# Kernel optimization log

Hardware: AMD Instinct MI355X
Metric: run time of the kernel (lower is better)

## Reference

```python
import jax, jax.numpy as jnp
import numpy as np

EMBED, HEADS, WIN, UP = 180, 6, 16, 4
HDIM = EMBED // HEADS

def _win_part(x, ws):
    # x: [B, H, W, C] -> [B*(H//ws)*(W//ws), ws, ws, C]
    B, H, W, C = x.shape
    x = x.reshape(B, H // ws, ws, W // ws, ws, C).transpose(0, 1, 3, 2, 4, 5)
    return x.reshape(-1, ws, ws, C)

def _win_rev(w, ws, H, W):
    # inverse of _win_part
    C = w.shape[-1]
    B = w.shape[0] // ((H // ws) * (W // ws))
    x = w.reshape(B, H // ws, W // ws, ws, ws, C).transpose(0, 1, 3, 2, 4, 5)
    return x.reshape(B, H, W, C)

def _ln(x, g, b):
    mu = x.mean(-1, keepdims=True)
    v = ((x - mu) ** 2).mean(-1, keepdims=True)
    return (x - mu) * jax.lax.rsqrt(v + 1e-5) * g + b

def _forward(gumbel_u, x, sel1_w, sel1_b, sel2_w, sel2_b, sel3_w, sel3_b,
             embed_w, embed_b, ln1_g, ln1_b, qkv_w, qkv_b, proj_w, proj_b,
             ln2_g, ln2_b, mlp1_w, mlp1_b, mlp2_w, mlp2_b, up_w, up_b):
    B, C, H, W = x.shape
    ws = H // 4                                     # 64 -> 16 tiles per image
    tiles = _win_part(x.transpose(0, 2, 3, 1), ws)  # [T, ws, ws, C]
    T = tiles.shape[0]
    # --- TileSelection (pooled MLP router) ---
    pooled = tiles.reshape(T, 8, ws // 8, 8, ws // 8, C).mean((2, 4)).reshape(T, 8 * 8 * C)
    f1 = pooled @ sel1_w + sel1_b
    f2 = jax.nn.relu(f1) @ sel2_w + sel2_b
    f3 = jax.nn.relu(f2) @ sel3_w + sel3_b          # [T, 2] routing logits
    # --- hard gumbel-softmax with straight-through estimator (tau=1) ---
    g = -jnp.log(-jnp.log(gumbel_u + 1e-10) + 1e-10)
    y_soft = jax.nn.softmax(f3 + g, axis=-1)
    y_hard = jax.nn.one_hot(jnp.argmax(y_soft, -1), 2, dtype=y_soft.dtype)
    pi = jax.lax.stop_gradient(y_hard - y_soft) + y_soft
    mask = pi[:, 1]                                 # 1 -> transformer expert
    # --- TR expert (SwinIR-style block, dense dispatch over all tiles) ---
    tok = tiles.reshape(T, ws * ws, C) @ embed_w + embed_b   # [T, 4096, 180]
    h = _ln(tok, ln1_g, ln1_b)
    hw = _win_part(h.reshape(T, ws, ws, EMBED), WIN).reshape(-1, WIN * WIN, EMBED)
    Nw, L = hw.shape[0], WIN * WIN
    qkv = (hw @ qkv_w + qkv_b).reshape(Nw, L, 3, HEADS, HDIM)
    q, k, v = qkv[:, :, 0], qkv[:, :, 1], qkv[:, :, 2]
    attn = jax.nn.softmax(jnp.einsum('nlhd,nmhd->nhlm', q, k) / np.sqrt(HDIM).astype(np.float32), axis=-1)
    av = jnp.einsum('nhlm,nmhd->nlhd', attn, v).reshape(Nw, L, EMBED)
    av = av @ proj_w + proj_b
    av = _win_rev(av.reshape(Nw, WIN, WIN, EMBED), WIN, ws, ws).reshape(T, ws * ws, EMBED)
    tok = tok + av
    h2 = _ln(tok, ln2_g, ln2_b)
    tok = tok + jax.nn.gelu(h2 @ mlp1_w + mlp1_b) @ mlp2_w + mlp2_b
    # pixelshuffle x4 upsample: 180 -> 3*4*4
    up = (tok @ up_w + up_b).reshape(T, ws, ws, UP, UP, C)
    up = up.transpose(0, 1, 3, 2, 4, 5).reshape(T, ws * UP, ws * UP, C)
    # --- cheap expert: bicubic x4 ---
    neg = jax.image.resize(tiles, (T, ws * UP, ws * UP, C), method='bicubic')
    # --- combine per-tile and reassemble ---
    m = mask[:, None, None, None]
    sr_tiles = m * up + (1.0 - m) * neg             # [T, 4ws, 4ws, C]
    sr = _win_rev(sr_tiles, H, H * UP, W * UP)      # [B, 4H, 4W, C]
    return sr.transpose(0, 3, 1, 2), f3, f2, f1

def setup_inputs() -> dict:
    key = jax.random.key(0)
    ks = jax.random.split(key, 16)
    B, C, H, W = 1, 3, 256, 256
    T = B * 16
    p = lambda k, s: jax.random.normal(k, s, jnp.float32) * 0.02
    return {
        'x': jax.random.normal(ks[0], (B, C, H, W), jnp.float32),
        'gumbel_u': jax.random.uniform(ks[1], (T, 2), jnp.float32),
        'sel1_w': p(ks[2], (192, 64)), 'sel1_b': jnp.zeros((64,), jnp.float32),
        'sel2_w': p(ks[3], (64, 32)), 'sel2_b': jnp.zeros((32,), jnp.float32),
        'sel3_w': p(ks[4], (32, 2)), 'sel3_b': jnp.zeros((2,), jnp.float32),
        'embed_w': p(ks[5], (3, EMBED)), 'embed_b': jnp.zeros((EMBED,), jnp.float32),
        'ln1_g': jnp.ones((EMBED,), jnp.float32), 'ln1_b': jnp.zeros((EMBED,), jnp.float32),
        'qkv_w': p(ks[6], (EMBED, 3 * EMBED)), 'qkv_b': jnp.zeros((3 * EMBED,), jnp.float32),
        'proj_w': p(ks[7], (EMBED, EMBED)), 'proj_b': jnp.zeros((EMBED,), jnp.float32),
        'ln2_g': jnp.ones((EMBED,), jnp.float32), 'ln2_b': jnp.zeros((EMBED,), jnp.float32),
        'mlp1_w': p(ks[8], (EMBED, 2 * EMBED)), 'mlp1_b': jnp.zeros((2 * EMBED,), jnp.float32),
        'mlp2_w': p(ks[9], (2 * EMBED, EMBED)), 'mlp2_b': jnp.zeros((EMBED,), jnp.float32),
        'up_w': p(ks[10], (EMBED, 3 * UP * UP)), 'up_b': jnp.zeros((3 * UP * UP,), jnp.float32),
    }

def reference(x, gumbel_u, sel1_w, sel1_b, sel2_w, sel2_b, sel3_w, sel3_b,
              embed_w, embed_b, ln1_g, ln1_b, qkv_w, qkv_b, proj_w, proj_b,
              ln2_g, ln2_b, mlp1_w, mlp1_b, mlp2_w, mlp2_b, up_w, up_b):
    return _forward(gumbel_u, x, sel1_w, sel1_b, sel2_w, sel2_b, sel3_w, sel3_b,
                    embed_w, embed_b, ln1_g, ln1_b, qkv_w, qkv_b, proj_w, proj_b,
                    ln2_g, ln2_b, mlp1_w, mlp1_b, mlp2_w, mlp2_b, up_w, up_b)
```

## Files before the change

### kernel.cpp

```cpp
#include <hip/hip_runtime.h>
#include <hip/hip_bf16.h>
#include <cstdint>

typedef __hip_bfloat16 bf16;
typedef __attribute__((ext_vector_type(8))) short short8;
typedef __attribute__((ext_vector_type(4))) short short4v;
typedef __attribute__((ext_vector_type(4))) float f32x4;
typedef __attribute__((ext_vector_type(2))) unsigned int uint2v;

__device__ __forceinline__ float bf2f(bf16 v) { return __bfloat162float(v); }
__device__ __forceinline__ bf16  f2bf(float v) { return __float2bfloat16(v); }
__device__ __forceinline__ float rbf(short s) {
  union { uint32_t u; float f; } c; c.u = ((uint32_t)(uint16_t)s) << 16; return c.f;
}
__device__ __forceinline__ uint32_t pack2(float a, float b) {
  bf16 x = f2bf(a), y = f2bf(b);
  return (uint32_t)(*(uint16_t*)&x) | ((uint32_t)(*(uint16_t*)&y) << 16);
}
__device__ __forceinline__ uint2v pack4(float a, float b, float c, float d) {
  uint2v r; r[0] = pack2(a, b); r[1] = pack2(c, d); return r;
}
__device__ __forceinline__ int swz(int row, int g) { return g ^ (row & 7); }

__device__ __forceinline__ int win_to_token(int m) {
  int n = m >> 8, l = m & 255;
  int t = n >> 4, win = n & 15;
  int wi = win >> 2, wj = win & 3;
  int u = l >> 4, v = l & 15;
  return (t << 12) | ((wi * 16 + u) << 6) | (wj * 16 + v);
}

__global__ __launch_bounds__(256) void k_packsel(
    const float* __restrict__ qkvw, const float* __restrict__ projw,
    const float* __restrict__ mlp1w, const float* __restrict__ mlp2w,
    const float* __restrict__ upw, const float* __restrict__ qkvb,
    bf16* __restrict__ Bt_qkv, bf16* __restrict__ Bt_proj,
    bf16* __restrict__ Bt_mlp1, bf16* __restrict__ Bt_mlp2,
    bf16* __restrict__ Bt_up, float* __restrict__ biasq,
    const float* __restrict__ x, const float* __restrict__ gu,
    const float* __restrict__ s1w, const float* __restrict__ s1b,
    const float* __restrict__ s2w, const float* __restrict__ s2b,
    const float* __restrict__ s3w, const float* __restrict__ s3b,
    float* __restrict__ f1o, float* __restrict__ f2o, float* __restrict__ f3o,
    float* __restrict__ maskp) {
  if (blockIdx.x < 1203) {
    int idx = blockIdx.x * 256 + threadIdx.x;
    const int e0 = 576 * 192, e1 = e0 + 192 * 192, e2 = e1 + 384 * 192,
              e3 = e2 + 192 * 384, e4 = e3 + 64 * 192, e5 = e4 + 576;
    if (idx < e0) {
      int np = idx / 192, k = idx % 192;
      int buf = np / 192, colp = np % 192;
      int hd = colp >> 5, dd = colp & 31;
      float v = 0.f;
      if (dd < 30 && k < 180) v = qkvw[(size_t)k * 540 + buf * 180 + hd * 30 + dd];
      Bt_qkv[idx] = f2bf(v);
    } else if (idx < e1) {
      int off = idx - e0; int n = off / 192, kp = off % 192;
      int hd = kp >> 5, dd = kp & 31;
      float v = (dd < 30 && n < 180) ? projw[(size_t)(hd * 30 + dd) * 180 + n] : 0.f;
      Bt_proj[off] = f2bf(v);
    } else if (idx < e2) {
      int off = idx - e1; int n = off / 192, k = off % 192;
      Bt_mlp1[off] = f2bf((k < 180 && n < 360) ? mlp1w[(size_t)k * 360 + n] : 0.f);
    } else if (idx < e3) {
      int off = idx - e2; int n = off / 384, k = off % 384;
      Bt_mlp2[off] = f2bf((k < 360 && n < 180) ? mlp2w[(size_t)k * 180 + n] : 0.f);
    } else if (idx < e4) {
      int off = idx - e3; int n = off / 192, k = off % 192;
      Bt_up[off] = f2bf((k < 180 && n < 48) ? upw[(size_t)k * 48 + n] : 0.f);
    } else if (idx < e5) {
      int np = idx - e4;
      int buf = np / 192, colp = np % 192;
      int hd = colp >> 5, dd = colp & 31;
      biasq[np] = (dd < 30) ? qkvb[buf * 180 + hd * 30 + dd] : 0.f;
    }
    return;
  }
  int t = blockIdx.x - 1203;
  int tid = threadIdx.x;
  int th = t >> 2, tw = t & 3;
  __shared__ float pooled[192];
  __shared__ float red[256];
  __shared__ float f1s[64], f2s[32], f3s[2];
  if (tid < 192) {
    int ch = tid % 3, j = (tid / 3) & 7, i = tid / 24;
    const float* xp = x + ch * 65536 + (th * 64 + i * 8) * 256 + (tw * 64 + j * 8);
    float s = 0.f;
#pragma unroll
    for (int a = 0; a < 8; ++a)
#pragma unroll
      for (int b = 0; b < 8; ++b) s += xp[a * 256 + b];
    pooled[tid] = s * (1.0f / 64.0f);
  }
  __syncthreads();
  {
    int o = tid & 63, part = tid >> 6;
    float s = 0.f;
    for (int k = part * 48; k < part * 48 + 48; ++k) s = fmaf(pooled[k], s1w[k * 64 + o], s);
    red[tid] = s;
  }
  __syncthreads();
  if (tid < 64) {
    float v = red[tid] + red[tid + 64] + red[tid + 128] + red[tid + 192] + s1b[tid];
    f1o[t * 64 + tid] = v;
    f1s[tid] = fmaxf(v, 0.f);
  }
  __syncthreads();
  {
    int o = tid & 31, part = tid >> 5;
    float s = 0.f;
    for (int k = part * 8; k < part * 8 + 8; ++k) s = fmaf(f1s[k], s2w[k * 32 + o], s);
    red[tid] = s;
  }
  __syncthreads();
  if (tid < 32) {
    float v = s2b[tid];
#pragma unroll
    for (int p = 0; p < 8; ++p) v += red[tid + p * 32];
    f2o[t * 32 + tid] = v;
    f2s[tid] = fmaxf(v, 0.f);
  }
  __syncthreads();
  if (tid < 2) {
    float s = s3b[tid];
    for (int k = 0; k < 32; ++k) s = fmaf(f2s[k], s3w[k * 2 + tid], s);
    f3o[t * 2 + tid] = s;
    f3s[tid] = s;
  }
  __syncthreads();
  if (tid == 0) {
    float g0 = -logf(-logf(gu[t * 2 + 0] + 1e-10f) + 1e-10f);
    float g1 = -logf(-logf(gu[t * 2 + 1] + 1e-10f) + 1e-10f);
    maskp[t] = (f3s[1] + g1 > f3s[0] + g0) ? 1.0f : 0.0f;
  }
}

__global__ __launch_bounds__(256) void k_embed(
    const float* __restrict__ x, const float* __restrict__ ew,
    const float* __restrict__ eb, const float* __restrict__ g1,
    const float* __restrict__ b1, bf16* __restrict__ tok,
    bf16* __restrict__ Aq) {
  int wrow = blockIdx.x * 4 + (threadIdx.x >> 6);
  int lane = threadIdx.x & 63;
  int token = win_to_token(wrow);
  int t = token >> 12, p = token & 4095;
  int r = p >> 6, c = p & 63;
  int gh = (t >> 2) * 64 + r, gw = (t & 3) * 64 + c;
  float x0 = x[gh * 256 + gw];
  float x1 = x[65536 + gh * 256 + gw];
  float x2 = x[131072 + gh * 256 + gw];
  float v[3];
  float s = 0.f, s2 = 0.f;
#pragma unroll
  for (int i = 0; i < 3; ++i) {
    int e = lane + i * 64;
    float vv = 0.f;
    if (e < 180) {
      vv = eb[e];
      vv = fmaf(x0, ew[e], vv);
      vv = fmaf(x1, ew[180 + e], vv);
      vv = fmaf(x2, ew[360 + e], vv);
      tok[(size_t)wrow * 180 + e] = f2bf(vv);
      s += vv; s2 = fmaf(vv, vv, s2);
    }
    v[i] = vv;
  }
#pragma unroll
  for (int off = 32; off; off >>= 1) { s += __shfl_xor(s, off); s2 += __shfl_xor(s2, off); }
  float mu = s * (1.f / 180.f);
  float rs = rsqrtf(s2 * (1.f / 180.f) - mu * mu + 1e-5f);
#pragma unroll
  for (int i = 0; i < 3; ++i) {
    int e = lane + i * 64;
    if (e < 192) {
      float a = (e < 180) ? ((v[i] - mu) * rs * g1[e] + b1[e]) : 0.f;
      Aq[(size_t)wrow * 192 + e] = f2bf(a);
    }
  }
}

__global__ __launch_bounds__(256) void k_qkv2(
    const bf16* __restrict__ A, const bf16* __restrict__ Bt,
    const float* __restrict__ biasq, bf16* __restrict__ Qp,
    bf16* __restrict__ Kp, bf16* __restrict__ Vp) {
  __shared__ bf16 Bs[2][64 * 192];
  const int tid = threadIdx.x;
  const int w = tid >> 6, l = tid & 63;
  const int lr = l & 15, lk = l >> 4;
  const int rbase = blockIdx.x * 128 + w * 32 + lr;

  short8 fa[2][6];
#pragma unroll
  for (int i = 0; i < 2; ++i) {
    const bf16* Ab = A + (size_t)(rbase + i * 16) * 192 + lk * 8;
#pragma unroll
    for (int ks = 0; ks < 6; ++ks) fa[i][ks] = *(const short8*)(Ab + ks * 32);
  }

  {
    const bf16* src = Bt;
#pragma unroll
    for (int it = 0; it < 6; ++it) {
      int c = tid + it * 256;
      int n = c / 24, g = c % 24;
      *(short8*)&Bs[0][n * 192 + swz(n, g) * 8] = *(const short8*)(src + n * 192 + g * 8);
    }
  }

  for (int nt = 0; nt < 9; ++nt) {
    __syncthreads();
    if (nt < 8) {
      const bf16* src = Bt + (size_t)(nt + 1) * 64 * 192;
      bf16* dstb = Bs[(nt + 1) & 1];
#pragma unroll
      for (int it = 0; it < 6; ++it) {
        int c = tid + it * 256;
        int n = c / 24, g = c % 24;
        *(short8*)&dstb[n * 192 + swz(n, g) * 8] = *(const short8*)(src + n * 192 + g * 8);
      }
    }
    const bf16* Bb = Bs[nt & 1];
    f32x4 acc[2][4];
#pragma unroll
    for (int i = 0; i < 2; ++i)
#pragma unroll
      for (int j = 0; j < 4; ++j) acc[i][j] = (f32x4){0.f, 0.f, 0.f, 0.f};
#pragma unroll
    for (int ks = 0; ks < 6; ++ks) {
      short8 fb[4];
#pragma unroll
      for (int j = 0; j < 4; ++j) {
        int rn = j * 16 + lr;
        fb[j] = *(const short8*)&Bb[rn * 192 + swz(rn, ks * 4 + lk) * 8];
      }
#pragma unroll
      for (int i = 0; i < 2; ++i)
#pragma unroll
        for (int j = 0; j < 4; ++j)
          acc[i][j] = __builtin_amdgcn_mfma_f32_16x16x32_bf16(fb[j], fa[i][ks], acc[i][j], 0, 0, 0);
    }
    bf16* dst = (nt < 3) ? Qp : (nt < 6) ? Kp : Vp;
    int c0 = (nt % 3) * 64;
#pragma unroll
    for (int i = 0; i < 2; ++i) {
      int row = rbase + i * 16;
#pragma unroll
      for (int j = 0; j < 4; ++j) {
        int np = nt * 64 + j * 16 + lk * 4;
        f32x4 bv = *(const f32x4*)&biasq[np];
        *(uint2v*)(dst + (size_t)row * 192 + c0 + j * 16 + lk * 4) =
            pack4(acc[i][j][0] + bv[0], acc[i][j][1] + bv[1],
                  acc[i][j][2] + bv[2], acc[i][j][3] + bv[3]);
      }
    }
  }
}

__global__ __launch_bounds__(256) void k_attn2(
    const bf16* __restrict__ Qp, const bf16* __restrict__ Kp,
    const bf16* __restrict__ Vp, bf16* __restrict__ av) {
  const int blk = blockIdx.x;
  const int win = blk / 6, hd = blk % 6;
  const int tid = threadIdx.x;
  const int w = tid >> 6, l = tid & 63;
  const int lr = l & 15, lk = l >> 4;
  const float scale = 0.18257418583505536f;

  __shared__ bf16 Ks[256][40];
  __shared__ bf16 Vs[32][264];
  __shared__ bf16 Ps[4][16][264];

  {
    const bf16* src = Kp + (size_t)(win * 256 + tid) * 192 + hd * 32;
#pragma unroll
    for (int c = 0; c < 4; ++c)
      *(short8*)&Ks[tid][c * 8] = *(const short8*)(src + c * 8);
  }
  {
    const bf16* src = Vp + (size_t)(win * 256 + tid) * 192 + hd * 32;
    short8 vv[4];
#pragma unroll
    for (int c = 0; c < 4; ++c) vv[c] = *(const short8*)(src + c * 8);
#pragma unroll
    for (int c = 0; c < 4; ++c)
#pragma unroll
      for (int e = 0; e < 8; ++e)
        *(short*)&Vs[c * 8 + e][tid] = vv[c][e];
  }
  __syncthreads();

  for (int qt = 0; qt < 4; ++qt) {
    const int qbase = qt * 64 + w * 16;
    short8 fq = *(const short8*)(Qp + (size_t)(win * 256 + qbase + lr) * 192 + hd * 32 + lk * 8);
    f32x4 accS[16];
#pragma unroll
    for (int kt = 0; kt < 16; ++kt) {
      short8 fk = *(const short8*)(&Ks[kt * 16 + lr][lk * 8]);
      accS[kt] = __builtin_amdgcn_mfma_f32_16x16x32_bf16(
          fk, fq, (f32x4){0.f, 0.f, 0.f, 0.f}, 0, 0, 0);
    }
    float mraw = -1e30f;
#pragma unroll
    for (int kt = 0; kt < 16; ++kt)
#pragma unroll
      for (int r = 0; r < 4; ++r) mraw = fmaxf(mraw, accS[kt][r]);
    mraw = fmaxf(mraw, __shfl_xor(mraw, 16));
    mraw = fmaxf(mraw, __shfl_xor(mraw, 32));
    const float mc = mraw * scale;
    float lsum = 0.f;
#pragma unroll
    for (int kt = 0; kt < 16; ++kt) {
      float p0 = __expf(fmaf(accS[kt][0], scale, -mc));
      float p1 = __expf(fmaf(accS[kt][1], scale, -mc));
      float p2 = __expf(fmaf(accS[kt][2], scale, -mc));
      float p3 = __expf(fmaf(accS[kt][3], scale, -mc));
      lsum += (p0 + p1) + (p2 + p3);
      *(uint32_t*)&Ps[w][lr][kt * 16 + lk * 4]     = pack2(p0, p1);
      *(uint32_t*)&Ps[w][lr][kt * 16 + lk * 4 + 2] = pack2(p2, p3);
    }
    lsum += __shfl_xor(lsum, 16);
    lsum += __shfl_xor(lsum, 32);
    __syncthreads();
    f32x4 accO0 = (f32x4){0.f, 0.f, 0.f, 0.f};
    f32x4 accO1 = (f32x4){0.f, 0.f, 0.f, 0.f};
#pragma unroll
    for (int ks = 0; ks < 8; ++ks) {
      short8 fp  = *(const short8*)(&Ps[w][lr][ks * 32 + lk * 8]);
      short8 fv0 = *(const short8*)(&Vs[lr][ks * 32 + lk * 8]);
      short8 fv1 = *(const short8*)(&Vs[16 + lr][ks * 32 + lk * 8]);
      accO0 = __builtin_amdgcn_mfma_f32_16x16x32_bf16(fv0, fp, accO0, 0, 0, 0);
      accO1 = __builtin_amdgcn_mfma_f32_16x16x32_bf16(fv1, fp, accO1, 0, 0, 0);
    }
    float invl = 1.f / lsum;
    bf16* avrow = av + (size_t)(win * 256 + qbase + lr) * 192 + hd * 32;
    *(uint2v*)(avrow + lk * 4) =
        pack4(accO0[0] * invl, accO0[1] * invl, accO0[2] * invl, accO0[3] * invl);
    *(uint2v*)(avrow + 16 + lk * 4) =
        pack4(accO1[0] * invl, accO1[1] * invl, accO1[2] * invl, accO1[3] * invl);
    __syncthreads();
  }
}

__global__ __launch_bounds__(256) void k_post(
    const bf16* __restrict__ av, const bf16* __restrict__ tok,
    const bf16* __restrict__ Btp, const float* __restrict__ pb,
    const float* __restrict__ g2, const float* __restrict__ b2,
    const bf16* __restrict__ Bt1, const float* __restrict__ b1m,
    const bf16* __restrict__ Bt2, const float* __restrict__ b2m,
    const bf16* __restrict__ Btu, const float* __restrict__ bu,
    bf16* __restrict__ up) {
  __shared__ bf16 Bs[2][64 * 192];
  __shared__ bf16 Hm[64 * 192];
  const int tid = threadIdx.x;
  const int w = tid >> 6, l = tid & 63;
  const int lr = l & 15, lk = l >> 4;
  const int row_l = w * 16 + lr;
  const int row_g = blockIdx.x * 64 + row_l;
  const int half = (lk & 1) * 4;

#define STAGE_A(srcp, dstb)                                               \
  {                                                                       \
    const bf16* _s = (srcp);                                              \
    bf16* _d = (dstb);                                                    \
    _Pragma("unroll")                                                     \
    for (int it = 0; it < 6; ++it) {                                      \
      int c = tid + it * 256;                                             \
      int n = c / 24, g = c % 24;                                         \
      *(short8*)&_d[n * 192 + swz(n, g) * 8] =                            \
          *(const short8*)(_s + (size_t)n * 192 + g * 8);                 \
    }                                                                     \
  }
#define STAGE_S(ntv, dstb)                                                \
  {                                                                       \
    bf16* _d = (dstb);                                                    \
    _Pragma("unroll")                                                     \
    for (int it = 0; it < 6; ++it) {                                      \
      int c = tid + it * 256;                                             \
      int n = c / 8, g = c % 8;                                           \
      *(short8*)&_d[n * 64 + swz(n, g) * 8] =                             \
          *(const short8*)(Bt2 + (size_t)n * 384 + (ntv) * 64 + g * 8);   \
    }                                                                     \
  }

  short8 fa[6];
  {
    const bf16* ab = av + (size_t)row_g * 192 + lk * 8;
#pragma unroll
    for (int ks = 0; ks < 6; ++ks) fa[ks] = *(const short8*)(ab + ks * 32);
  }

  f32x4 t2v[3][4];

  STAGE_A(Btp, Bs[0]);

#pragma unroll
  for (int nt = 0; nt < 3; ++nt) {
    __syncthreads();
    if (nt < 2) { STAGE_A(Btp + (size_t)(nt + 1) * 64 * 192, Bs[(nt + 1) & 1]); }
    else        { STAGE_A(Bt1, Bs[1]); }
    const bf16* Bb = Bs[nt & 1];
    f32x4 acc[4];
#pragma unroll
    for (int j = 0; j < 4; ++j) acc[j] = (f32x4){0.f, 0.f, 0.f, 0.f};
#pragma unroll
    for (int ks = 0; ks < 6; ++ks) {
      short8 fb[4];
#pragma unroll
      for (int j = 0; j < 4; ++j) {
        int rn = j * 16 + lr;
        fb[j] = *(const short8*)&Bb[rn * 192 + swz(rn, ks * 4 + lk) * 8];
      }
#pragma unroll
      for (int j = 0; j < 4; ++j)
        acc[j] = __builtin_amdgcn_mfma_f32_16x16x32_bf16(fb[j], fa[ks], acc[j], 0, 0, 0);
    }
#pragma unroll
    for (int j = 0; j < 4; ++j) {
      int n = nt * 64 + j * 16 + lk * 4;
      if (n < 180) {
        f32x4 bv = *(const f32x4*)&pb[n];
        short4v tv = *(const short4v*)(tok + (size_t)row_g * 180 + n);
#pragma unroll
        for (int q = 0; q < 4; ++q) t2v[nt][j][q] = acc[j][q] + bv[q] + rbf(tv[q]);
      } else {
        t2v[nt][j] = (f32x4){0.f, 0.f, 0.f, 0.f};
      }
    }
  }

  {
    float s = 0.f, s2 = 0.f;
#pragma unroll
    for (int nt = 0; nt < 3; ++nt)
#pragma unroll
      for (int j = 0; j < 4; ++j)
#pragma unroll
        for (int q = 0; q < 4; ++q) { float v = t2v[nt][j][q]; s += v; s2 = fmaf(v, v, s2); }
    s += __shfl_xor(s, 16);  s += __shfl_xor(s, 32);
    s2 += __shfl_xor(s2, 16); s2 += __shfl_xor(s2, 32);
    float mu = s * (1.f / 180.f);
    float rs = rsqrtf(s2 * (1.f / 180.f) - mu * mu + 1e-5f);
#pragma unroll
    for (int nt = 0; nt < 3; ++nt)
#pragma unroll
      for (int j = 0; j < 4; ++j) {
        int n = nt * 64 + j * 16 + lk * 4;
        float h[4] = {0.f, 0.f, 0.f, 0.f};
        if (n < 180) {
          f32x4 gv = *(const f32x4*)&g2[n];
          f32x4 bv = *(const f32x4*)&b2[n];
#pragma unroll
          for (int q = 0; q < 4; ++q) h[q] = (t2v[nt][j][q] - mu) * rs * gv[q] + bv[q];
        }
        int g = nt * 8 + j * 2 + (lk >> 1);
        *(uint2v*)&Hm[row_l * 192 + swz(row_l, g) * 8 + half] = pack4(h[0], h[1], h[2], h[3]);
      }
  }

  short8 fh[6];
  f32x4 acc2[3][4];
#pragma unroll
  for (int t = 0; t < 3; ++t)
#pragma unroll
    for (int j = 0; j < 4; ++j) acc2[t][j] = (f32x4){0.f, 0.f, 0.f, 0.f};

#pragma unroll
  for (int nt = 0; nt < 6; ++nt) {
    __syncthreads();
    STAGE_S(nt, Bs[0]);
    if (nt == 0) {
#pragma unroll
      for (int ks = 0; ks < 6; ++ks)
        fh[ks] = *(const short8*)&Hm[row_l * 192 + swz(row_l, ks * 4 + lk) * 8];
    }
    {
      const bf16* Bb = Bs[1];
      f32x4 acc1[4];
#pragma unroll
      for (int j = 0; j < 4; ++j) acc1[j] = (f32x4){0.f, 0.f, 0.f, 0.f};
#pragma unroll
      for (int ks = 0; ks < 6; ++ks) {
        short8 fb[4];
#pragma unroll
        for (int j = 0; j < 4; ++j) {
          int rn = j * 16 + lr;
          fb[j] = *(const short8*)&Bb[rn * 192 + swz(rn, ks * 4 + lk) * 8];
        }
#pragma unroll
        for (int j = 0; j < 4; ++j)
          acc1[j] = __builtin_amdgcn_mfma_f32_16x16x32_bf16(fb[j], fh[ks], acc1[j], 0, 0, 0);
      }
#pragma unroll
      for (int j = 0; j < 4; ++j) {
        int n = nt * 64 + j * 16 + lk * 4;
        float m4[4] = {0.f, 0.f, 0.f, 0.f};
        if (n < 360) {
          f32x4 bv = *(const f32x4*)&b1m[n];
#pragma unroll
          for (int q = 0; q < 4; ++q) {
            float v = acc1[j][q] + bv[q];
            float u = 0.7978845608028654f * (v + 0.044715f * v * v * v);
            m4[q] = v / (1.f + __expf(-2.f * u));
          }
        }
        int g = j * 2 + (lk >> 1);
        *(uint2v*)&Hm[row_l * 192 + swz(row_l, g) * 8 + half] = pack4(m4[0], m4[1], m4[2], m4[3]);
      }
    }
    __syncthreads();
    if (nt < 5) { STAGE_A(Bt1 + (size_t)(nt + 1) * 64 * 192, Bs[1]); }
    else        { STAGE_A(Btu, Bs[1]); }
    {
      short8 fm[2];
#pragma unroll
      for (int s = 0; s < 2; ++s)
        fm[s] = *(const short8*)&Hm[row_l * 192 + swz(row_l, s * 4 + lk) * 8];
#pragma unroll
      for (int s = 0; s < 2; ++s)
#pragma unroll
        for (int t = 0; t < 3; ++t)
#pragma unroll
          for (int j = 0; j < 4; ++j) {
            int rn = t * 64 + j * 16 + lr;
            short8 fb2 = *(const short8*)&Bs[0][rn * 64 + swz(rn, s * 4 + lk) * 8];
            acc2[t][j] = __builtin_amdgcn_mfma_f32_16x16x32_bf16(fb2, fm[s], acc2[t][j], 0, 0, 0);
          }
    }
  }

  __syncthreads();
#pragma unroll
  for (int t = 0; t < 3; ++t)
#pragma unroll
    for (int j = 0; j < 4; ++j) {
      int n = t * 64 + j * 16 + lk * 4;
      float o4[4] = {0.f, 0.f, 0.f, 0.f};
      if (n < 180) {
        f32x4 bv = *(const f32x4*)&b2m[n];
#pragma unroll
        for (int q = 0; q < 4; ++q) o4[q] = acc2[t][j][q] + bv[q] + t2v[t][j][q];
      }
      int g = t * 8 + j * 2 + (lk >> 1);
      *(uint2v*)&Hm[row_l * 192 + swz(row_l, g) * 8 + half] = pack4(o4[0], o4[1], o4[2], o4[3]);
    }
  __syncthreads();

  short8 ft[6];
#pragma unroll
  for (int ks = 0; ks < 6; ++ks)
    ft[ks] = *(const short8*)&Hm[row_l * 192 + swz(row_l, ks * 4 + lk) * 8];
  f32x4 acc3[3];
#pragma unroll
  for (int j = 0; j < 3; ++j) acc3[j] = (f32x4){0.f, 0.f, 0.f, 0.f};
#pragma unroll
  for (int ks = 0; ks < 6; ++ks) {
    short8 fb[3];
#pragma unroll
    for (int j = 0; j < 3; ++j) {
      int rn = j * 16 + lr;
      fb[j] = *(const short8*)&Bs[1][rn * 192 + swz(rn, ks * 4 + lk) * 8];
    }
#pragma unroll
    for (int j = 0; j < 3; ++j)
      acc3[j] = __builtin_amdgcn_mfma_f32_16x16x32_bf16(fb[j], ft[ks], acc3[j], 0, 0, 0);
  }
#pragma unroll
  for (int j = 0; j < 3; ++j) {
    int n = j * 16 + lk * 4;
    f32x4 bv = *(const f32x4*)&bu[n];
    *(uint2v*)(up + (size_t)row_g * 48 + n) =
        pack4(acc3[j][0] + bv[0], acc3[j][1] + bv[1], acc3[j][2] + bv[2], acc3[j][3] + bv[3]);
  }
#undef STAGE_A
#undef STAGE_S
}

__device__ const float c_cubw[4][4] = {
    {-0.0439453125f, 0.3896484375f, 0.7275390625f, -0.0732421875f},
    {-0.0068359375f, 0.0908203125f, 0.9638671875f, -0.0478515625f},
    {-0.0478515625f, 0.9638671875f, 0.0908203125f, -0.0068359375f},
    {-0.0732421875f, 0.7275390625f, 0.3896484375f, -0.0439453125f},
};

__device__ __forceinline__ void cubw(int r, int ph, float* w, int& base) {
  base = r + ((ph < 2) ? -2 : -1);
  float sum = 0.f;
#pragma unroll
  for (int i = 0; i < 4; ++i) {
    int idx = base + i;
    float wi = (idx >= 0 && idx < 64) ? c_cubw[ph][i] : 0.f;
    w[i] = wi; sum += wi;
  }
  float inv = 1.f / sum;
#pragma unroll
  for (int i = 0; i < 4; ++i) w[i] *= inv;
}

__global__ __launch_bounds__(256) void k_blend(
    const bf16* __restrict__ up, const float* __restrict__ x,
    const float* __restrict__ maskp, float* __restrict__ sr) {
  int idx = blockIdx.x * 256 + threadIdx.x;
  int ch = idx >> 20;
  int rem = idx & 1048575;
  int gR = rem >> 10, gC = rem & 1023;
  int th = gR >> 8, tw = gC >> 8;
  int t = th * 4 + tw;
  int R = gR & 255, C = gC & 255;
  int r = R >> 2, a = R & 3, c = C >> 2, b = C & 3;
  float m = maskp[t];
  float outv;
  if (m > 0.5f) {
    int wi = r >> 4, u = r & 15, wj = c >> 4, v = c & 15;
    int wrow = (t * 16 + wi * 4 + wj) * 256 + u * 16 + v;
    outv = bf2f(up[(size_t)wrow * 48 + a * 12 + b * 3 + ch]);
  } else {
    float wy[4], wx[4];
    int yb, xb;
    cubw(r, a, wy, yb);
    cubw(c, b, wx, xb);
    const float* xc = x + ch * 65536;
    float neg = 0.f;
#pragma unroll
    for (int i = 0; i < 4; ++i) {
      int yi = yb + i;
      if (yi < 0 || yi > 63) continue;
      float rowsum = 0.f;
#pragma unroll
      for (int j = 0; j < 4; ++j) {
        int xj = xb + j;
        if (xj < 0 || xj > 63) continue;
        rowsum = fmaf(wx[j], xc[(th * 64 + yi) * 256 + tw * 64 + xj], rowsum);
      }
      neg = fmaf(wy[i], rowsum, neg);
    }
    outv = neg;
  }
  sr[idx] = outv;
}

extern "C" void kernel_launch(void* const* d_in, const int* in_sizes, int n_in,
                              void* d_out, int out_size, void* d_ws, size_t ws_size,
                              hipStream_t stream) {
  const float* x     = (const float*)d_in[0];
  const float* gu    = (const float*)d_in[1];
  const float* s1w   = (const float*)d_in[2];
  const float* s1b   = (const float*)d_in[3];
  const float* s2w   = (const float*)d_in[4];
  const float* s2b   = (const float*)d_in[5];
  const float* s3w   = (const float*)d_in[6];
  const float* s3b   = (const float*)d_in[7];
  const float* ew    = (const float*)d_in[8];
  const float* ebias = (const float*)d_in[9];
  const float* ln1g  = (const float*)d_in[10];
  const float* ln1b  = (const float*)d_in[11];
  const float* qkvw  = (const float*)d_in[12];
  const float* qkvb  = (const float*)d_in[13];
  const float* projw = (const float*)d_in[14];
  const float* projb = (const float*)d_in[15];
  const float* ln2g  = (const float*)d_in[16];
  const float* ln2b  = (const float*)d_in[17];
  const float* mlp1w = (const float*)d_in[18];
  const float* mlp1b = (const float*)d_in[19];
  const float* mlp2w = (const float*)d_in[20];
  const float* mlp2b = (const float*)d_in[21];
  const float* upw   = (const float*)d_in[22];
  const float* upb   = (const float*)d_in[23];

  float* out = (float*)d_out;
  float* sr  = out;
  float* f3o = out + 3145728;
  float* f2o = f3o + 32;
  float* f1o = f2o + 512;

  char* ws = (char*)d_ws;
  bf16* tok  = (bf16*)(ws);
  bf16* ABuf = (bf16*)(ws + 23592960);
  bf16* Qp   = (bf16*)(ws + 48758784);
  bf16* Kp   = (bf16*)(ws + 73924608);
  bf16* Vp   = (bf16*)(ws + 99090432);
  float* maskp   = (float*)(ws + 124256256);
  bf16* Bt_qkv  = (bf16*)(ws + 124256320);
  bf16* Bt_proj = (bf16*)(ws + 124477504);
  bf16* Bt_mlp1 = (bf16*)(ws + 124551232);
  bf16* Bt_mlp2 = (bf16*)(ws + 124698688);
  bf16* Bt_up   = (bf16*)(ws + 124846144);
  float* biasq  = (float*)(ws + 124870720);
  bf16* up      = (bf16*)(ws + 124873088);
  bf16* av = ABuf;

  k_packsel<<<1219, 256, 0, stream>>>(qkvw, projw, mlp1w, mlp2w, upw, qkvb,
                                      Bt_qkv, Bt_proj, Bt_mlp1, Bt_mlp2, Bt_up, biasq,
                                      x, gu, s1w, s1b, s2w, s2b, s3w, s3b,
                                      f1o, f2o, f3o, maskp);
  k_embed<<<16384, 256, 0, stream>>>(x, ew, ebias, ln1g, ln1b, tok, ABuf);
  k_qkv2<<<512, 256, 0, stream>>>(ABuf, Bt_qkv, biasq, Qp, Kp, Vp);
  k_attn2<<<1536, 256, 0, stream>>>(Qp, Kp, Vp, av);
  k_post<<<1024, 256, 0, stream>>>(av, tok, Bt_proj, projb, ln2g, ln2b,
                                   Bt_mlp1, mlp1b, Bt_mlp2, mlp2b, Bt_up, upb, up);
  k_blend<<<12288, 256, 0, stream>>>(up, x, maskp, sr);
}
```

Before: 215.0 us.

## Use 1024-thread blocks for QKV and post GEMM kernels to amortize weight staging

The QKV and post-attention kernels are relaunched with 1024-thread blocks covering 256 rows each, so every staged weight tile in shared memory is reused by 16 waves instead of 4. The QKV kernel also drops from 32 to 16 rows per wave, which halves its per-wave accumulator register use. The aim is to cut redundant global-to-LDS weight traffic per row. The cost is 256 blocks with one block per CU on a large device. The post kernel's Hm buffer also grows to 256×192 bf16 (about 96 KB), which raises LDS pressure and limits occupancy.

```diff
diff --git a/kernel.cpp b/kernel.cpp
--- a/kernel.cpp
+++ b/kernel.cpp
@@ -179,7 +179,7 @@
   }
 }
 
-__global__ __launch_bounds__(256) void k_qkv2(
+__global__ __launch_bounds__(1024, 1) void k_qkv3(
     const bf16* __restrict__ A, const bf16* __restrict__ Bt,
     const float* __restrict__ biasq, bf16* __restrict__ Qp,
     bf16* __restrict__ Kp, bf16* __restrict__ Vp) {
@@ -187,24 +187,18 @@
   const int tid = threadIdx.x;
   const int w = tid >> 6, l = tid & 63;
   const int lr = l & 15, lk = l >> 4;
-  const int rbase = blockIdx.x * 128 + w * 32 + lr;
-
-  short8 fa[2][6];
-#pragma unroll
-  for (int i = 0; i < 2; ++i) {
-    const bf16* Ab = A + (size_t)(rbase + i * 16) * 192 + lk * 8;
-#pragma unroll
-    for (int ks = 0; ks < 6; ++ks) fa[i][ks] = *(const short8*)(Ab + ks * 32);
-  }
-
+  const int row = blockIdx.x * 256 + w * 16 + lr;
+
+  short8 fa[6];
   {
-    const bf16* src = Bt;
-#pragma unroll
-    for (int it = 0; it < 6; ++it) {
-      int c = tid + it * 256;
-      int n = c / 24, g = c % 24;
-      *(short8*)&Bs[0][n * 192 + swz(n, g) * 8] = *(const short8*)(src + n * 192 + g * 8);
-    }
+    const bf16* Ab = A + (size_t)row * 192 + lk * 8;
+#pragma unroll
+    for (int ks = 0; ks < 6; ++ks) fa[ks] = *(const short8*)(Ab + ks * 32);
+  }
+
+  for (int c = tid; c < 1536; c += 1024) {
+    int n = c / 24, g = c % 24;
+    *(short8*)&Bs[0][n * 192 + swz(n, g) * 8] = *(const short8*)(Bt + (size_t)n * 192 + g * 8);
   }
 
   for (int nt = 0; nt < 9; ++nt) {
@@ -212,19 +206,15 @@
     if (nt < 8) {
       const bf16* src = Bt + (size_t)(nt + 1) * 64 * 192;
       bf16* dstb = Bs[(nt + 1) & 1];
-#pragma unroll
-      for (int it = 0; it < 6; ++it) {
-        int c = tid + it * 256;
+      for (int c = tid; c < 1536; c += 1024) {
         int n = c / 24, g = c % 24;
-        *(short8*)&dstb[n * 192 + swz(n, g) * 8] = *(const short8*)(src + n * 192 + g * 8);
+        *(short8*)&dstb[n * 192 + swz(n, g) * 8] = *(const short8*)(src + (size_t)n * 192 + g * 8);
       }
     }
     const bf16* Bb = Bs[nt & 1];
-    f32x4 acc[2][4];
-#pragma unroll
-    for (int i = 0; i < 2; ++i)
-#pragma unroll
-      for (int j = 0; j < 4; ++j) acc[i][j] = (f32x4){0.f, 0.f, 0.f, 0.f};
+    f32x4 acc[4];
+#pragma unroll
+    for (int j = 0; j < 4; ++j) acc[j] = (f32x4){0.f, 0.f, 0.f, 0.f};
 #pragma unroll
     for (int ks = 0; ks < 6; ++ks) {
       short8 fb[4];
@@ -234,24 +224,17 @@
         fb[j] = *(const short8*)&Bb[rn * 192 + swz(rn, ks * 4 + lk) * 8];
       }
 #pragma unroll
-      for (int i = 0; i < 2; ++i)
-#pragma unroll
-        for (int j = 0; j < 4; ++j)
-          acc[i][j] = __builtin_amdgcn_mfma_f32_16x16x32_bf16(fb[j], fa[i][ks], acc[i][j], 0, 0, 0);
+      for (int j = 0; j < 4; ++j)
+        acc[j] = __builtin_amdgcn_mfma_f32_16x16x32_bf16(fb[j], fa[ks], acc[j], 0, 0, 0);
     }
     bf16* dst = (nt < 3) ? Qp : (nt < 6) ? Kp : Vp;
     int c0 = (nt % 3) * 64;
 #pragma unroll
-    for (int i = 0; i < 2; ++i) {
-      int row = rbase + i * 16;
-#pragma unroll
-      for (int j = 0; j < 4; ++j) {
-        int np = nt * 64 + j * 16 + lk * 4;
-        f32x4 bv = *(const f32x4*)&biasq[np];
-        *(uint2v*)(dst + (size_t)row * 192 + c0 + j * 16 + lk * 4) =
-            pack4(acc[i][j][0] + bv[0], acc[i][j][1] + bv[1],
-                  acc[i][j][2] + bv[2], acc[i][j][3] + bv[3]);
-      }
+    for (int j = 0; j < 4; ++j) {
+      int np = nt * 64 + j * 16 + lk * 4;
+      f32x4 bv = *(const f32x4*)&biasq[np];
+      *(uint2v*)(dst + (size_t)row * 192 + c0 + j * 16 + lk * 4) =
+          pack4(acc[j][0] + bv[0], acc[j][1] + bv[1], acc[j][2] + bv[2], acc[j][3] + bv[3]);
     }
   }
 }
@@ -341,7 +324,7 @@
   }
 }
 
-__global__ __launch_bounds__(256) void k_post(
+__global__ __launch_bounds__(1024, 1) void k_post(
     const bf16* __restrict__ av, const bf16* __restrict__ tok,
     const bf16* __restrict__ Btp, const float* __restrict__ pb,
     const float* __restrict__ g2, const float* __restrict__ b2,
@@ -350,21 +333,19 @@
     const bf16* __restrict__ Btu, const float* __restrict__ bu,
     bf16* __restrict__ up) {
   __shared__ bf16 Bs[2][64 * 192];
-  __shared__ bf16 Hm[64 * 192];
+  __shared__ bf16 Hm[256 * 192];
   const int tid = threadIdx.x;
   const int w = tid >> 6, l = tid & 63;
   const int lr = l & 15, lk = l >> 4;
   const int row_l = w * 16 + lr;
-  const int row_g = blockIdx.x * 64 + row_l;
+  const int row_g = blockIdx.x * 256 + row_l;
   const int half = (lk & 1) * 4;
 
 #define STAGE_A(srcp, dstb)                                               \
   {                                                                       \
     const bf16* _s = (srcp);                                              \
     bf16* _d = (dstb);                                                    \
-    _Pragma("unroll")                                                     \
-    for (int it = 0; it < 6; ++it) {                                      \
-      int c = tid + it * 256;                                             \
+    for (int c = tid; c < 1536; c += 1024) {                              \
       int n = c / 24, g = c % 24;                                         \
       *(short8*)&_d[n * 192 + swz(n, g) * 8] =                            \
           *(const short8*)(_s + (size_t)n * 192 + g * 8);                 \
@@ -373,9 +354,7 @@
 #define STAGE_S(ntv, dstb)                                                \
   {                                                                       \
     bf16* _d = (dstb);                                                    \
-    _Pragma("unroll")                                                     \
-    for (int it = 0; it < 6; ++it) {                                      \
-      int c = tid + it * 256;                                             \
+    for (int c = tid; c < 1536; c += 1024) {                              \
       int n = c / 8, g = c % 8;                                           \
       *(short8*)&_d[n * 64 + swz(n, g) * 8] =                             \
           *(const short8*)(Bt2 + (size_t)n * 384 + (ntv) * 64 + g * 8);   \
@@ -693,9 +672,9 @@
                                       x, gu, s1w, s1b, s2w, s2b, s3w, s3b,
                                       f1o, f2o, f3o, maskp);
   k_embed<<<16384, 256, 0, stream>>>(x, ew, ebias, ln1g, ln1b, tok, ABuf);
-  k_qkv2<<<512, 256, 0, stream>>>(ABuf, Bt_qkv, biasq, Qp, Kp, Vp);
+  k_qkv3<<<256, 1024, 0, stream>>>(ABuf, Bt_qkv, biasq, Qp, Kp, Vp);
   k_attn2<<<1536, 256, 0, stream>>>(Qp, Kp, Vp, av);
-  k_post<<<1024, 256, 0, stream>>>(av, tok, Bt_proj, projb, ln2g, ln2b,
+  k_post<<<256, 1024, 0, stream>>>(av, tok, Bt_proj, projb, ln2g, ln2b,
                                    Bt_mlp1, mlp1b, Bt_mlp2, mlp2b, Bt_up, upb, up);
   k_blend<<<12288, 256, 0, stream>>>(up, x, maskp, sr);
 }
```

Result: no change. 217.6 us (+1.2%).
